# Kernel optimization log

Hardware: AMD Instinct MI355X
Metric: run time of the kernel (lower is better)

Reference implementation:

```python
import jax, jax.numpy as jnp
import numpy as np

N_NODES = 50000
N_EDGES = 800000  # random edges, guaranteed no self loops; self loops appended explicitly
D_FEAT = 128
N_LAYERS = 4


def setup_inputs() -> dict:
    key = jax.random.key(0)
    k1, k2, k3, k4 = jax.random.split(key, 4)
    src = jax.random.randint(k1, (N_EDGES,), 0, N_NODES)
    # offset in [1, N-1] guarantees dst != src (module removes self loops anyway)
    off = jax.random.randint(k2, (N_EDGES,), 1, N_NODES)
    dst = (src + off) % N_NODES
    # add_self_loop: append i->i for every node (module does this every layer;
    # with drop_edge p=0 the per-layer graph is identical, so build once)
    loops = jnp.arange(N_NODES)
    src = jnp.concatenate([src, loops])
    dst = jnp.concatenate([dst, loops])
    in_feat = jax.random.normal(k3, (N_NODES, D_FEAT), jnp.float32)
    Ws = jax.random.normal(k4, (N_LAYERS, D_FEAT, D_FEAT), jnp.float32) / np.sqrt(D_FEAT)
    bs = jnp.zeros((N_LAYERS, D_FEAT), jnp.float32)
    return {"in_feat": in_feat, "Ws": Ws, "bs": bs, "src": src, "dst": dst}


def reference(in_feat, Ws, bs, src, dst):
    # JKNet: L x [dropout(p=0) -> GraphConv(norm='both') -> LeakyReLU], then JK max.
    N = in_feat.shape[0]
    ones = jnp.ones(src.shape[0], in_feat.dtype)
    deg_out = jax.ops.segment_sum(ones, src, num_segments=N)  # out-degree (src norm)
    deg_in = jax.ops.segment_sum(ones, dst, num_segments=N)   # in-degree  (dst norm)
    norm_src = jnp.maximum(deg_out, 1.0) ** -0.5
    norm_dst = jnp.maximum(deg_in, 1.0) ** -0.5

    feat_list = [in_feat]
    x = in_feat
    for l in range(Ws.shape[0]):
        h = x * norm_src[:, None]
        agg = jax.ops.segment_sum(h[src], dst, num_segments=N)  # [N, d] sparse aggregation
        h = agg * norm_dst[:, None]
        h = h @ Ws[l] + bs[l]
        x = jax.nn.leaky_relu(h, negative_slope=0.01)  # nn.LeakyReLU default
        feat_list.append(x)

    # Jumping-knowledge max pooling over layer outputs (torch.max values)
    return jnp.max(jnp.stack(feat_list, axis=-1), axis=-1)
```

## Files before the change

kernel.cpp:

```cpp
#include <hip/hip_runtime.h>
#include <cstdint>

#define D 128
#define MAXDEG 64

typedef __attribute__((ext_vector_type(8))) short bf16x8;
typedef __attribute__((ext_vector_type(4))) float f32x4;

__device__ __forceinline__ unsigned short f2b(float f) {
  unsigned u = __float_as_uint(f);
  return (unsigned short)((u + 0x7fffu + ((u >> 16) & 1u)) >> 16);
}
__device__ __forceinline__ float blo(unsigned u) { return __uint_as_float(u << 16); }
__device__ __forceinline__ float bhi(unsigned u) { return __uint_as_float(u & 0xffff0000u); }

__global__ __launch_bounds__(256) void init_kernel(int* __restrict__ cursor,
    int* __restrict__ dego, int N) {
  int i = blockIdx.x * 256 + threadIdx.x;
  if (i < N) {
    cursor[i] = i * MAXDEG;
    dego[i] = 0;
  }
}

__global__ __launch_bounds__(256) void fill_deg(const int* __restrict__ src,
    const int* __restrict__ dst, int* __restrict__ cursor,
    int* __restrict__ esrc, int* __restrict__ dego, int Er) {
  int e = blockIdx.x * 256 + threadIdx.x;
  if (e < Er) {
    int s = src[e];
    int d = dst[e];
    int slot = atomicAdd(cursor + d, 1);
    esrc[slot] = s;
    atomicAdd(dego + s, 1);
  }
}

__global__ __launch_bounds__(256) void norm_kernel(const int* __restrict__ dego,
    const int* __restrict__ cursor, float* __restrict__ ns,
    float* __restrict__ nd, int N) {
  int i = blockIdx.x * 256 + threadIdx.x;
  if (i < N) {
    ns[i] = rsqrtf((float)(dego[i] + 1));
    nd[i] = rsqrtf((float)(cursor[i] - i * MAXDEG + 1));
  }
}

template<bool INF32>
__global__ __launch_bounds__(256, 4) void gemm_mfma(const float* __restrict__ xf,
    const unsigned short* __restrict__ xb, const float* __restrict__ nsrc,
    const float* __restrict__ W, unsigned short* __restrict__ zout, int N) {
  __shared__ unsigned short Wt[D * D];
  for (int i = threadIdx.x; i < D * D; i += 256) {
    int k = i >> 7;
    int c = i & 127;
    Wt[(c * D + k) ^ ((c & 7) << 3)] = f2b(W[i]);
  }
  __syncthreads();

  int wave = threadIdx.x >> 6;
  int lane = threadIdx.x & 63;
  int r16 = lane & 15;
  int kgrp = lane >> 4;
  int rw = blockIdx.x * 64 + wave * 16;

  f32x4 acc[8] = {};
  int gr = rw + r16;
  if (gr >= N) gr = N - 1;

  #pragma unroll
  for (int ks = 0; ks < 4; ++ks) {
    int k0 = ks * 32 + kgrp * 8;
    bf16x8 a;
    if (INF32) {
      const float4* p = (const float4*)(xf + (size_t)gr * D + k0);
      float4 lo = p[0], hi = p[1];
      a[0] = (short)f2b(lo.x); a[1] = (short)f2b(lo.y);
      a[2] = (short)f2b(lo.z); a[3] = (short)f2b(lo.w);
      a[4] = (short)f2b(hi.x); a[5] = (short)f2b(hi.y);
      a[6] = (short)f2b(hi.z); a[7] = (short)f2b(hi.w);
    } else {
      a = *(const bf16x8*)(xb + (size_t)gr * D + k0);
    }
    #pragma unroll
    for (int ct = 0; ct < 8; ++ct) {
      int c = ct * 16 + r16;
      bf16x8 b = *(const bf16x8*)(Wt + ((c * D + k0) ^ ((c & 7) << 3)));
      acc[ct] = __builtin_amdgcn_mfma_f32_16x16x32_bf16(a, b, acc[ct], 0, 0, 0);
    }
  }

  #pragma unroll
  for (int q = 0; q < 4; ++q) {
    int row = rw + kgrp * 4 + q;
    if (row < N) {
      float ns = nsrc[row];
      #pragma unroll
      for (int ct = 0; ct < 8; ++ct) {
        zout[(size_t)row * D + ct * 16 + r16] = f2b(acc[ct][q] * ns);
      }
    }
  }
}

struct Acc8 {
  float a0, a1, a2, a3, a4, a5, a6, a7;
  __device__ __forceinline__ void zero() {
    a0 = a1 = a2 = a3 = a4 = a5 = a6 = a7 = 0.f;
  }
  __device__ __forceinline__ void add(uint4 v) {
    a0 += blo(v.x); a1 += bhi(v.x); a2 += blo(v.y); a3 += bhi(v.y);
    a4 += blo(v.z); a5 += bhi(v.z); a6 += blo(v.w); a7 += bhi(v.w);
  }
};

__device__ __forceinline__ void epilogue(const Acc8& a, int row, int cg,
    float nd, float4 bv0, float4 bv1, const float* __restrict__ jk_in,
    unsigned short* __restrict__ xb_out, float* __restrict__ jk_out,
    int write_x) {
  float4 o0, o1;
  o0.x = nd * a.a0 + bv0.x; o0.y = nd * a.a1 + bv0.y;
  o0.z = nd * a.a2 + bv0.z; o0.w = nd * a.a3 + bv0.w;
  o1.x = nd * a.a4 + bv1.x; o1.y = nd * a.a5 + bv1.y;
  o1.z = nd * a.a6 + bv1.z; o1.w = nd * a.a7 + bv1.w;
  o0.x = o0.x > 0.f ? o0.x : 0.01f * o0.x;
  o0.y = o0.y > 0.f ? o0.y : 0.01f * o0.y;
  o0.z = o0.z > 0.f ? o0.z : 0.01f * o0.z;
  o0.w = o0.w > 0.f ? o0.w : 0.01f * o0.w;
  o1.x = o1.x > 0.f ? o1.x : 0.01f * o1.x;
  o1.y = o1.y > 0.f ? o1.y : 0.01f * o1.y;
  o1.z = o1.z > 0.f ? o1.z : 0.01f * o1.z;
  o1.w = o1.w > 0.f ? o1.w : 0.01f * o1.w;
  if (write_x) {
    uint4 px;
    px.x = (unsigned)f2b(o0.x) | ((unsigned)f2b(o0.y) << 16);
    px.y = (unsigned)f2b(o0.z) | ((unsigned)f2b(o0.w) << 16);
    px.z = (unsigned)f2b(o1.x) | ((unsigned)f2b(o1.y) << 16);
    px.w = (unsigned)f2b(o1.z) | ((unsigned)f2b(o1.w) << 16);
    ((uint4*)xb_out)[(size_t)row * 16 + cg] = px;
  }
  size_t o4 = (size_t)row * 32 + cg * 2;
  float4 m0 = ((const float4*)jk_in)[o4];
  float4 m1 = ((const float4*)jk_in)[o4 + 1];
  m0.x = fmaxf(m0.x, o0.x); m0.y = fmaxf(m0.y, o0.y);
  m0.z = fmaxf(m0.z, o0.z); m0.w = fmaxf(m0.w, o0.w);
  m1.x = fmaxf(m1.x, o1.x); m1.y = fmaxf(m1.y, o1.y);
  m1.z = fmaxf(m1.z, o1.z); m1.w = fmaxf(m1.w, o1.w);
  ((float4*)jk_out)[o4] = m0;
  ((float4*)jk_out)[o4 + 1] = m1;
}

__global__ __launch_bounds__(256, 8) void gather_kernel(
    const unsigned short* __restrict__ z, const int* __restrict__ row_end,
    const int* __restrict__ esrc, const float* __restrict__ ndst,
    const float* __restrict__ bias, const float* __restrict__ jk_in,
    unsigned short* __restrict__ xb_out, float* __restrict__ jk_out,
    int N, int write_x) {
  int t = blockIdx.x * 256 + threadIdx.x;
  int pr = t >> 4;
  int r0 = pr * 2;
  if (r0 >= N) return;
  int r1 = r0 + 1;
  bool has1 = (r1 < N);
  int cg = t & 15;
  const uint4* zp = (const uint4*)z;

  int b0 = r0 * MAXDEG;
  int d0 = row_end[r0] - b0;
  int b1 = has1 ? r1 * MAXDEG : 0;
  int d1 = has1 ? row_end[r1] - b1 : 0;

  Acc8 A0, A1;
  A0.zero(); A1.zero();
  A0.add(zp[(size_t)r0 * 16 + cg]);
  if (has1) A1.add(zp[(size_t)r1 * 16 + cg]);

  int dm = d0 > d1 ? d0 : d1;
  int k = 0;
  for (; k + 1 < dm; k += 2) {
    if (k + 1 < d0) {
      int2 s = *(const int2*)(esrc + b0 + k);
      uint4 v0 = zp[(size_t)s.x * 16 + cg];
      uint4 v1 = zp[(size_t)s.y * 16 + cg];
      A0.add(v0); A0.add(v1);
    } else if (k < d0) {
      A0.add(zp[(size_t)esrc[b0 + k] * 16 + cg]);
    }
    if (k + 1 < d1) {
      int2 s = *(const int2*)(esrc + b1 + k);
      uint4 v0 = zp[(size_t)s.x * 16 + cg];
      uint4 v1 = zp[(size_t)s.y * 16 + cg];
      A1.add(v0); A1.add(v1);
    } else if (k < d1) {
      A1.add(zp[(size_t)esrc[b1 + k] * 16 + cg]);
    }
  }
  if (k < dm) {
    if (k < d0) A0.add(zp[(size_t)esrc[b0 + k] * 16 + cg]);
    if (k < d1) A1.add(zp[(size_t)esrc[b1 + k] * 16 + cg]);
  }

  float4 bv0 = ((const float4*)bias)[cg * 2];
  float4 bv1 = ((const float4*)bias)[cg * 2 + 1];
  epilogue(A0, r0, cg, ndst[r0], bv0, bv1, jk_in, xb_out, jk_out, write_x);
  if (has1)
    epilogue(A1, r1, cg, ndst[r1], bv0, bv1, jk_in, xb_out, jk_out, write_x);
}

extern "C" void kernel_launch(void* const* d_in, const int* in_sizes, int n_in,
                              void* d_out, int out_size, void* d_ws, size_t ws_size,
                              hipStream_t stream) {
  const float* in_feat = (const float*)d_in[0];
  const float* Ws = (const float*)d_in[1];
  const float* bs = (const float*)d_in[2];
  const int* src = (const int*)d_in[3];
  const int* dst = (const int*)d_in[4];
  int N = in_sizes[0] / D;
  int L = in_sizes[2] / D;
  int E = in_sizes[3];
  float* out = (float*)d_out;

  int Er = E - N;
  if (Er < 0) Er = E;

  char* p = (char*)d_ws;
  int* dego   = (int*)p;   p += (size_t)N * 4;
  int* cursor = (int*)p;   p += (size_t)N * 4;
  int* esrc   = (int*)p;   p += (size_t)N * MAXDEG * 4;
  float* nsrc = (float*)p; p += (size_t)N * 4;
  float* ndst = (float*)p; p += (size_t)N * 4;
  unsigned short* z  = (unsigned short*)p; p += (size_t)N * D * 2;
  unsigned short* xb = (unsigned short*)p;

  init_kernel<<<(N + 255) / 256, 256, 0, stream>>>(cursor, dego, N);
  fill_deg<<<(Er + 255) / 256, 256, 0, stream>>>(src, dst, cursor, esrc, dego, Er);
  norm_kernel<<<(N + 255) / 256, 256, 0, stream>>>(dego, cursor, nsrc, ndst, N);

  int mb = (N + 63) / 64;
  int gb = (int)((((long long)((N + 1) / 2)) * 16 + 255) / 256);
  for (int l = 0; l < L; ++l) {
    const float* jk_in = (l == 0) ? in_feat : out;
    if (l == 0) {
      gemm_mfma<true><<<mb, 256, 0, stream>>>(in_feat, nullptr, nsrc,
                                              Ws, z, N);
    } else {
      gemm_mfma<false><<<mb, 256, 0, stream>>>(nullptr, xb, nsrc,
                                               Ws + (size_t)l * D * D, z, N);
    }
    gather_kernel<<<gb, 256, 0, stream>>>(z, cursor, esrc, ndst,
                                          bs + (size_t)l * D, jk_in, xb, out,
                                          N, (l + 1 < L) ? 1 : 0);
  }
}
```

Measured before the change: 298.1 us.

## Sort rows by in-degree buckets and keep JK running max in bf16

Adds a degree histogram, a scan and a scatter that build an order of rows grouped by in-degree, so each gather wavefront processes rows of similar degree and divergence is reduced. The gather now handles one row per 16 threads with 4-way unrolled neighbour loads instead of two interleaved rows. The intermediate jumping-knowledge max is stored in bf16 rather than fp32, which halves that traffic but loses precision in the running max. Costs are three extra small setup kernels and less locality in the output writes, since rows are visited in permuted order.

```diff
diff --git a/kernel.cpp b/kernel.cpp
--- a/kernel.cpp
+++ b/kernel.cpp
@@ -15,12 +15,13 @@
 __device__ __forceinline__ float bhi(unsigned u) { return __uint_as_float(u & 0xffff0000u); }
 
 __global__ __launch_bounds__(256) void init_kernel(int* __restrict__ cursor,
-    int* __restrict__ dego, int N) {
+    int* __restrict__ dego, int* __restrict__ bcnt, int N) {
   int i = blockIdx.x * 256 + threadIdx.x;
   if (i < N) {
     cursor[i] = i * MAXDEG;
     dego[i] = 0;
   }
+  if (i < 64) bcnt[i] = 0;
 }
 
 __global__ __launch_bounds__(256) void fill_deg(const int* __restrict__ src,
@@ -36,14 +37,61 @@
   }
 }
 
-__global__ __launch_bounds__(256) void norm_kernel(const int* __restrict__ dego,
+__global__ __launch_bounds__(256) void norm_hist(const int* __restrict__ dego,
     const int* __restrict__ cursor, float* __restrict__ ns,
-    float* __restrict__ nd, int N) {
-  int i = blockIdx.x * 256 + threadIdx.x;
+    float* __restrict__ nd, int* __restrict__ bcnt, int N) {
+  __shared__ int h[64];
+  int t = threadIdx.x;
+  if (t < 64) h[t] = 0;
+  __syncthreads();
+  int i = blockIdx.x * 256 + t;
   if (i < N) {
+    int din = cursor[i] - i * MAXDEG;
     ns[i] = rsqrtf((float)(dego[i] + 1));
-    nd[i] = rsqrtf((float)(cursor[i] - i * MAXDEG + 1));
-  }
+    nd[i] = rsqrtf((float)(din + 1));
+    int d = din > 63 ? 63 : din;
+    atomicAdd(&h[d], 1);
+  }
+  __syncthreads();
+  if (t < 64 && h[t]) atomicAdd(bcnt + t, h[t]);
+}
+
+__global__ __launch_bounds__(64) void bucket_scan(const int* __restrict__ bcnt,
+    int* __restrict__ bcur) {
+  __shared__ int tmp[64];
+  int t = threadIdx.x;
+  int v = bcnt[t];
+  tmp[t] = v;
+  __syncthreads();
+  #pragma unroll
+  for (int off = 1; off < 64; off <<= 1) {
+    int u = (t >= off) ? tmp[t - off] : 0;
+    __syncthreads();
+    tmp[t] += u;
+    __syncthreads();
+  }
+  bcur[t] = tmp[t] - v;
+}
+
+__global__ __launch_bounds__(256) void bucket_scatter(const int* __restrict__ cursor,
+    int* __restrict__ bcur, int* __restrict__ order, int N) {
+  __shared__ int h[64];
+  __shared__ int bbase[64];
+  int t = threadIdx.x;
+  if (t < 64) h[t] = 0;
+  __syncthreads();
+  int i = blockIdx.x * 256 + t;
+  int d = 0, lp = 0;
+  bool ok = (i < N);
+  if (ok) {
+    int din = cursor[i] - i * MAXDEG;
+    d = din > 63 ? 63 : din;
+    lp = atomicAdd(&h[d], 1);
+  }
+  __syncthreads();
+  if (t < 64) bbase[t] = h[t] ? atomicAdd(bcur + t, h[t]) : 0;
+  __syncthreads();
+  if (ok) order[bbase[d] + lp] = i;
 }
 
 template<bool INF32>
@@ -114,15 +162,48 @@
   }
 };
 
-__device__ __forceinline__ void epilogue(const Acc8& a, int row, int cg,
-    float nd, float4 bv0, float4 bv1, const float* __restrict__ jk_in,
-    unsigned short* __restrict__ xb_out, float* __restrict__ jk_out,
-    int write_x) {
+template<bool INJ32, bool OUTJ32>
+__global__ __launch_bounds__(256, 8) void gather_kernel(
+    const unsigned short* __restrict__ z, const int* __restrict__ order,
+    const int* __restrict__ row_end, const int* __restrict__ esrc,
+    const float* __restrict__ ndst, const float* __restrict__ bias,
+    const float* __restrict__ jkinf, const unsigned short* __restrict__ jkinb,
+    unsigned short* __restrict__ xb_out, float* __restrict__ jkoutf,
+    unsigned short* __restrict__ jkoutb, int N, int write_x) {
+  int t = blockIdx.x * 256 + threadIdx.x;
+  int pr = t >> 4;
+  if (pr >= N) return;
+  int row = order[pr];
+  int cg = t & 15;
+  const uint4* zp = (const uint4*)z;
+
+  int b = row * MAXDEG;
+  int e = row_end[row];
+  Acc8 A;
+  A.zero();
+  A.add(zp[(size_t)row * 16 + cg]);
+
+  int j = b;
+  for (; j + 3 < e; j += 4) {
+    int4 s = *(const int4*)(esrc + j);
+    uint4 v0 = zp[(size_t)s.x * 16 + cg];
+    uint4 v1 = zp[(size_t)s.y * 16 + cg];
+    uint4 v2 = zp[(size_t)s.z * 16 + cg];
+    uint4 v3 = zp[(size_t)s.w * 16 + cg];
+    A.add(v0); A.add(v1); A.add(v2); A.add(v3);
+  }
+  for (; j < e; ++j) {
+    A.add(zp[(size_t)esrc[j] * 16 + cg]);
+  }
+
+  float nd = ndst[row];
+  float4 bv0 = ((const float4*)bias)[cg * 2];
+  float4 bv1 = ((const float4*)bias)[cg * 2 + 1];
   float4 o0, o1;
-  o0.x = nd * a.a0 + bv0.x; o0.y = nd * a.a1 + bv0.y;
-  o0.z = nd * a.a2 + bv0.z; o0.w = nd * a.a3 + bv0.w;
-  o1.x = nd * a.a4 + bv1.x; o1.y = nd * a.a5 + bv1.y;
-  o1.z = nd * a.a6 + bv1.z; o1.w = nd * a.a7 + bv1.w;
+  o0.x = nd * A.a0 + bv0.x; o0.y = nd * A.a1 + bv0.y;
+  o0.z = nd * A.a2 + bv0.z; o0.w = nd * A.a3 + bv0.w;
+  o1.x = nd * A.a4 + bv1.x; o1.y = nd * A.a5 + bv1.y;
+  o1.z = nd * A.a6 + bv1.z; o1.w = nd * A.a7 + bv1.w;
   o0.x = o0.x > 0.f ? o0.x : 0.01f * o0.x;
   o0.y = o0.y > 0.f ? o0.y : 0.01f * o0.y;
   o0.z = o0.z > 0.f ? o0.z : 0.01f * o0.z;
@@ -131,6 +212,7 @@
   o1.y = o1.y > 0.f ? o1.y : 0.01f * o1.y;
   o1.z = o1.z > 0.f ? o1.z : 0.01f * o1.z;
   o1.w = o1.w > 0.f ? o1.w : 0.01f * o1.w;
+
   if (write_x) {
     uint4 px;
     px.x = (unsigned)f2b(o0.x) | ((unsigned)f2b(o0.y) << 16);
@@ -139,72 +221,31 @@
     px.w = (unsigned)f2b(o1.z) | ((unsigned)f2b(o1.w) << 16);
     ((uint4*)xb_out)[(size_t)row * 16 + cg] = px;
   }
-  size_t o4 = (size_t)row * 32 + cg * 2;
-  float4 m0 = ((const float4*)jk_in)[o4];
-  float4 m1 = ((const float4*)jk_in)[o4 + 1];
+
+  float4 m0, m1;
+  if (INJ32) {
+    m0 = ((const float4*)jkinf)[(size_t)row * 32 + cg * 2];
+    m1 = ((const float4*)jkinf)[(size_t)row * 32 + cg * 2 + 1];
+  } else {
+    uint4 mj = ((const uint4*)jkinb)[(size_t)row * 16 + cg];
+    m0.x = blo(mj.x); m0.y = bhi(mj.x); m0.z = blo(mj.y); m0.w = bhi(mj.y);
+    m1.x = blo(mj.z); m1.y = bhi(mj.z); m1.z = blo(mj.w); m1.w = bhi(mj.w);
+  }
   m0.x = fmaxf(m0.x, o0.x); m0.y = fmaxf(m0.y, o0.y);
   m0.z = fmaxf(m0.z, o0.z); m0.w = fmaxf(m0.w, o0.w);
   m1.x = fmaxf(m1.x, o1.x); m1.y = fmaxf(m1.y, o1.y);
   m1.z = fmaxf(m1.z, o1.z); m1.w = fmaxf(m1.w, o1.w);
-  ((float4*)jk_out)[o4] = m0;
-  ((float4*)jk_out)[o4 + 1] = m1;
-}
-
-__global__ __launch_bounds__(256, 8) void gather_kernel(
-    const unsigned short* __restrict__ z, const int* __restrict__ row_end,
-    const int* __restrict__ esrc, const float* __restrict__ ndst,
-    const float* __restrict__ bias, const float* __restrict__ jk_in,
-    unsigned short* __restrict__ xb_out, float* __restrict__ jk_out,
-    int N, int write_x) {
-  int t = blockIdx.x * 256 + threadIdx.x;
-  int pr = t >> 4;
-  int r0 = pr * 2;
-  if (r0 >= N) return;
-  int r1 = r0 + 1;
-  bool has1 = (r1 < N);
-  int cg = t & 15;
-  const uint4* zp = (const uint4*)z;
-
-  int b0 = r0 * MAXDEG;
-  int d0 = row_end[r0] - b0;
-  int b1 = has1 ? r1 * MAXDEG : 0;
-  int d1 = has1 ? row_end[r1] - b1 : 0;
-
-  Acc8 A0, A1;
-  A0.zero(); A1.zero();
-  A0.add(zp[(size_t)r0 * 16 + cg]);
-  if (has1) A1.add(zp[(size_t)r1 * 16 + cg]);
-
-  int dm = d0 > d1 ? d0 : d1;
-  int k = 0;
-  for (; k + 1 < dm; k += 2) {
-    if (k + 1 < d0) {
-      int2 s = *(const int2*)(esrc + b0 + k);
-      uint4 v0 = zp[(size_t)s.x * 16 + cg];
-      uint4 v1 = zp[(size_t)s.y * 16 + cg];
-      A0.add(v0); A0.add(v1);
-    } else if (k < d0) {
-      A0.add(zp[(size_t)esrc[b0 + k] * 16 + cg]);
-    }
-    if (k + 1 < d1) {
-      int2 s = *(const int2*)(esrc + b1 + k);
-      uint4 v0 = zp[(size_t)s.x * 16 + cg];
-      uint4 v1 = zp[(size_t)s.y * 16 + cg];
-      A1.add(v0); A1.add(v1);
-    } else if (k < d1) {
-      A1.add(zp[(size_t)esrc[b1 + k] * 16 + cg]);
-    }
-  }
-  if (k < dm) {
-    if (k < d0) A0.add(zp[(size_t)esrc[b0 + k] * 16 + cg]);
-    if (k < d1) A1.add(zp[(size_t)esrc[b1 + k] * 16 + cg]);
-  }
-
-  float4 bv0 = ((const float4*)bias)[cg * 2];
-  float4 bv1 = ((const float4*)bias)[cg * 2 + 1];
-  epilogue(A0, r0, cg, ndst[r0], bv0, bv1, jk_in, xb_out, jk_out, write_x);
-  if (has1)
-    epilogue(A1, r1, cg, ndst[r1], bv0, bv1, jk_in, xb_out, jk_out, write_x);
+  if (OUTJ32) {
+    ((float4*)jkoutf)[(size_t)row * 32 + cg * 2] = m0;
+    ((float4*)jkoutf)[(size_t)row * 32 + cg * 2 + 1] = m1;
+  } else {
+    uint4 pm;
+    pm.x = (unsigned)f2b(m0.x) | ((unsigned)f2b(m0.y) << 16);
+    pm.y = (unsigned)f2b(m0.z) | ((unsigned)f2b(m0.w) << 16);
+    pm.z = (unsigned)f2b(m1.x) | ((unsigned)f2b(m1.y) << 16);
+    pm.w = (unsigned)f2b(m1.z) | ((unsigned)f2b(m1.w) << 16);
+    ((uint4*)jkoutb)[(size_t)row * 16 + cg] = pm;
+  }
 }
 
 extern "C" void kernel_launch(void* const* d_in, const int* in_sizes, int n_in,
@@ -223,32 +264,50 @@
   int Er = E - N;
   if (Er < 0) Er = E;
 
+  int nb = (N + 255) / 256;
+
   char* p = (char*)d_ws;
   int* dego   = (int*)p;   p += (size_t)N * 4;
   int* cursor = (int*)p;   p += (size_t)N * 4;
+  int* order  = (int*)p;   p += (size_t)N * 4;
+  int* bcnt   = (int*)p;   p += 64 * 4;
+  int* bcur   = (int*)p;   p += 64 * 4;
   int* esrc   = (int*)p;   p += (size_t)N * MAXDEG * 4;
   float* nsrc = (float*)p; p += (size_t)N * 4;
   float* ndst = (float*)p; p += (size_t)N * 4;
-  unsigned short* z  = (unsigned short*)p; p += (size_t)N * D * 2;
-  unsigned short* xb = (unsigned short*)p;
-
-  init_kernel<<<(N + 255) / 256, 256, 0, stream>>>(cursor, dego, N);
+  unsigned short* z   = (unsigned short*)p; p += (size_t)N * D * 2;
+  unsigned short* xb  = (unsigned short*)p; p += (size_t)N * D * 2;
+  unsigned short* jkb = (unsigned short*)p;
+
+  init_kernel<<<nb, 256, 0, stream>>>(cursor, dego, bcnt, N);
   fill_deg<<<(Er + 255) / 256, 256, 0, stream>>>(src, dst, cursor, esrc, dego, Er);
-  norm_kernel<<<(N + 255) / 256, 256, 0, stream>>>(dego, cursor, nsrc, ndst, N);
+  norm_hist<<<nb, 256, 0, stream>>>(dego, cursor, nsrc, ndst, bcnt, N);
+  bucket_scan<<<1, 64, 0, stream>>>(bcnt, bcur);
+  bucket_scatter<<<nb, 256, 0, stream>>>(cursor, bcur, order, N);
 
   int mb = (N + 63) / 64;
-  int gb = (int)((((long long)((N + 1) / 2)) * 16 + 255) / 256);
+  int gb = (int)(((long long)N * 16 + 255) / 256);
   for (int l = 0; l < L; ++l) {
-    const float* jk_in = (l == 0) ? in_feat : out;
     if (l == 0) {
-      gemm_mfma<true><<<mb, 256, 0, stream>>>(in_feat, nullptr, nsrc,
-                                              Ws, z, N);
+      gemm_mfma<true><<<mb, 256, 0, stream>>>(in_feat, nullptr, nsrc, Ws, z, N);
     } else {
       gemm_mfma<false><<<mb, 256, 0, stream>>>(nullptr, xb, nsrc,
                                                Ws + (size_t)l * D * D, z, N);
     }
-    gather_kernel<<<gb, 256, 0, stream>>>(z, cursor, esrc, ndst,
-                                          bs + (size_t)l * D, jk_in, xb, out,
-                                          N, (l + 1 < L) ? 1 : 0);
-  }
-}
+    const float* bias = bs + (size_t)l * D;
+    int wx = (l + 1 < L) ? 1 : 0;
+    if (l == 0 && L == 1) {
+      gather_kernel<true, true><<<gb, 256, 0, stream>>>(z, order, cursor, esrc,
+          ndst, bias, in_feat, nullptr, xb, out, nullptr, N, wx);
+    } else if (l == 0) {
+      gather_kernel<true, false><<<gb, 256, 0, stream>>>(z, order, cursor, esrc,
+          ndst, bias, in_feat, nullptr, xb, nullptr, jkb, N, wx);
+    } else if (l == L - 1) {
+      gather_kernel<false, true><<<gb, 256, 0, stream>>>(z, order, cursor, esrc,
+          ndst, bias, nullptr, jkb, xb, out, nullptr, N, wx);
+    } else {
+      gather_kernel<false, false><<<gb, 256, 0, stream>>>(z, order, cursor, esrc,
+          ndst, bias, nullptr, jkb, xb, nullptr, jkb, N, wx);
+    }
+  }
+}
```

New measurement: 339.3 us. 1.14x slower.
